# Optimization experiments

Hardware: AMD Instinct MI355X
Metric: run time of the kernel (lower is better)

Reference implementation:

```python
import jax, jax.numpy as jnp
import numpy as np

N, B, H, C, NF = 200000, 100, 128, 3, 128


def setup_inputs() -> dict:
    key = jax.random.key(0)
    ks = jax.random.split(key, 12)
    def w(k, shape, s=0.05):
        return jax.random.normal(k, shape, jnp.float32) * s
    return dict(
        node_feat=w(ks[0], (N, NF), 1.0),
        coord=w(ks[1], (N, 3), 1.0),
        virtual_node_feat=w(ks[2], (B, NF, C), 1.0),
        virtual_coord=w(ks[3], (B, 3, C), 1.0),
        data_batch=jnp.sort(jax.random.randint(ks[4], (N,), 0, B)),
        We1=w(ks[5], (2 * NF + 1, H)), be1=jnp.zeros((H,), jnp.float32),
        We2=w(ks[6], (H, H)), be2=jnp.zeros((H,), jnp.float32),
        Wc1=w(ks[7], (H, H)), bc1=jnp.zeros((H,), jnp.float32),
        Wc2=w(ks[8], (H, 1), 0.001),  # xavier gain=0.001 layer, no bias
        Wn1=w(ks[9], (2 * H, H)), bn1=jnp.zeros((H,), jnp.float32),
        Wn2=w(ks[10], (H, H)), bn2=jnp.zeros((H,), jnp.float32),
    )


def _segment_mean(x, idx, num_segments):
    # x: [N, d1, d2] -> [num_segments, d1, d2]; mean over nodes of each graph
    sums = jax.ops.segment_sum(x, idx, num_segments=num_segments)
    counts = jax.ops.segment_sum(jnp.ones((x.shape[0],), x.dtype), idx,
                                 num_segments=num_segments)
    return sums / jnp.maximum(counts, 1.0)[:, None, None]


def reference(node_feat, coord, virtual_node_feat, virtual_coord, data_batch,
              We1, be1, We2, be2, Wc1, bc1, Wc2, Wn1, bn1, Wn2, bn2):
    silu = jax.nn.silu
    n, nf = node_feat.shape
    nb, _, c = virtual_coord.shape

    # gather: real node -> its graph's virtual nodes
    diff = virtual_coord[data_batch] - coord[:, :, None]            # [N,3,C]
    radial = jnp.linalg.norm(diff, axis=1)                          # [N,C]

    # edge model (work in [N,C,feat] layout to avoid permutes)
    feat_R = jnp.broadcast_to(node_feat[:, None, :], (n, c, nf))    # [N,C,NF]
    feat_V = virtual_node_feat[data_batch].transpose(0, 2, 1)       # [N,C,NF]
    e_in = jnp.concatenate([feat_R, feat_V, radial[:, :, None]], axis=-1)
    m = silu(e_in @ We1 + be1)
    m = silu(m @ We2 + be2)                                         # [N,C,H]

    # coord model: per (node, virtual-channel) scalar weight
    s = silu(m @ Wc1 + bc1) @ Wc2                                   # [N,C,1]
    trans = diff * s[:, :, 0][:, None, :]                           # [N,3,C]
    virtual_coord = virtual_coord + _segment_mean(trans, data_batch, nb)

    # node model on virtual nodes
    agg = _segment_mean(m, data_batch, nb)                          # [B,C,H]
    n_in = jnp.concatenate([virtual_node_feat.transpose(0, 2, 1), agg], axis=-1)
    h = silu(n_in @ Wn1 + bn1) @ Wn2 + bn2                          # [B,C,H]
    virtual_node_feat = virtual_node_feat + h.transpose(0, 2, 1)    # residual

    return virtual_node_feat, virtual_coord
```

## Files before the change

### kernel.cpp

```cpp
#include <hip/hip_runtime.h>
#include <hip/hip_bf16.h>
#include <math.h>

#define NNODES 200000
#define NGRAPH 100
#define HD     128
#define NCH    3
#define BN     64
#define EROWS  (BN*NCH)
#define ESTR   136

typedef short short8 __attribute__((ext_vector_type(8)));
typedef float f32x4  __attribute__((ext_vector_type(4)));

#define MFMA_16x16x32(a,b,c) __builtin_amdgcn_mfma_f32_16x16x32_bf16((a),(b),(c),0,0,0)

__device__ __forceinline__ float bf2f(unsigned short u) {
    return __uint_as_float(((unsigned int)u) << 16);
}
__device__ __forceinline__ unsigned short f2bf(float f) {
    return (unsigned short)((__float_as_uint(f) + 0x8000u) >> 16);
}
__device__ __forceinline__ float silu_f(float x) {
    return x * __builtin_amdgcn_rcpf(1.0f + __expf(-x));
}

__global__ void prep_kernel(const float* __restrict__ We1,
                            const float* __restrict__ We2,
                            const float* __restrict__ Wc1,
                            const float* __restrict__ be1,
                            const float* __restrict__ be2,
                            const float* __restrict__ bc1,
                            const float* __restrict__ Wc2,
                            const float* __restrict__ vnf,
                            unsigned short* __restrict__ w1r,
                            unsigned short* __restrict__ w2r,
                            unsigned short* __restrict__ wc1r,
                            float* __restrict__ Q,
                            float* __restrict__ wlast,
                            float* __restrict__ be1f,
                            float* __restrict__ be2f,
                            float* __restrict__ bc1f,
                            float* __restrict__ wc2f) {
    int bid = blockIdx.x;
    if (bid < 192) {
        int t = bid * 256 + threadIdx.x;
        int m  = t / 16384;
        int e  = t % 16384;
        int j  = e & 7;
        int l  = (e >> 3) & 63;
        int ks = (e >> 9) & 3;
        int ct = e >> 11;
        int row = ks * 32 + (l >> 4) * 8 + j;
        int col = ct * 16 + (l & 15);
        const float*    src = (m == 0) ? We1 : ((m == 1) ? We2 : Wc1);
        unsigned short* dst = (m == 0) ? w1r : ((m == 1) ? w2r : wc1r);
        dst[e] = f2bf(src[row * 128 + col]);
        if (t < 128) {
            wlast[t] = We1[256 * 128 + t];
            be1f[t]  = be1[t];
            be2f[t]  = be2[t];
            bc1f[t]  = bc1[t];
            wc2f[t]  = Wc2[t];
        }
    } else {
        int bc = bid - 192;
        int b = bc / NCH, c = bc % NCH;
        int t = threadIdx.x;
        __shared__ float v[128];
        if (t < 128) v[t] = vnf[(b * 128 + t) * 3 + c];
        __syncthreads();
        if (t < 128) {
            float s = 0.0f;
            for (int k = 0; k < 128; ++k)
                s += v[k] * We1[(128 + k) * 128 + t];
            Q[(b * 3 + c) * 128 + t] = s;
        }
    }
}

__global__ __launch_bounds__(256, 2) void egcl_main(
    const float* __restrict__ node_feat,
    const float* __restrict__ coord,
    const float* __restrict__ vcoord,
    const int*   __restrict__ batch,
    const unsigned short* __restrict__ w1r,
    const unsigned short* __restrict__ w2r,
    const unsigned short* __restrict__ wc1r,
    const float* __restrict__ Q,
    const float* __restrict__ wlast,
    const float* __restrict__ be1f,
    const float* __restrict__ be2f,
    const float* __restrict__ bc1f,
    const float* __restrict__ wc2f,
    float* __restrict__ aggsum,
    float* __restrict__ transsum,
    float* __restrict__ cnt)
{
    __shared__ __align__(16) unsigned short e_buf[EROWS * ESTR];
    __shared__ float s_s[EROWS];
    __shared__ unsigned short sbatch[BN];
    __shared__ unsigned short sseg_start[BN + 1];
    __shared__ unsigned short sseg_b[BN];
    __shared__ int snseg;

    const int tid   = threadIdx.x;
    const int wave  = tid >> 6;
    const int lane  = tid & 63;
    const int lrow  = lane & 15;
    const int lkb   = (lane >> 4) * 8;
    const int rq    = (lane >> 4) * 4;
    const int node0 = blockIdx.x * BN;

    if (tid < BN) {
        int n = node0 + tid;
        int b = batch[n];
        sbatch[tid] = (unsigned short)b;
        int prev = (tid > 0) ? batch[n - 1] : -1;
        unsigned long long mask = __ballot(b != prev);
        int ns = __popcll(mask);
        if (b != prev) {
            int idx = __popcll(mask & ((1ull << tid) - 1ull));
            sseg_start[idx] = (unsigned short)tid;
            sseg_b[idx]     = (unsigned short)b;
        }
        if (tid == 0) { sseg_start[ns] = BN; snseg = ns; }
        float cx = coord[n * 3 + 0];
        float cy = coord[n * 3 + 1];
        float cz = coord[n * 3 + 2];
        for (int c = 0; c < 3; ++c) {
            float dx = vcoord[b * 9 + 0 * 3 + c] - cx;
            float dy = vcoord[b * 9 + 1 * 3 + c] - cy;
            float dz = vcoord[b * 9 + 2 * 3 + c] - cz;
            f32x4 pad;
            pad[0] = dx; pad[1] = dy; pad[2] = dz;
            pad[3] = sqrtf(dx * dx + dy * dy + dz * dz);
            *(f32x4*)&e_buf[(c * 64 + tid) * ESTR + 128] = pad;
        }
    }
    __syncthreads();
    const int nseg = snseg;

    f32x4 acc1[8] = {};
    {
        const float* arow = node_feat + (size_t)(node0 + wave * 16 + lrow) * 128;
        for (int ks = 0; ks < 4; ++ks) {
            f32x4 x0 = *(const f32x4*)(arow + ks * 32 + lkb);
            f32x4 x1 = *(const f32x4*)(arow + ks * 32 + lkb + 4);
            short8 af;
            af[0] = (short)f2bf(x0[0]); af[1] = (short)f2bf(x0[1]);
            af[2] = (short)f2bf(x0[2]); af[3] = (short)f2bf(x0[3]);
            af[4] = (short)f2bf(x1[0]); af[5] = (short)f2bf(x1[1]);
            af[6] = (short)f2bf(x1[2]); af[7] = (short)f2bf(x1[3]);
            for (int ct = 0; ct < 8; ++ct) {
                short8 bfg = *(const short8*)(w1r + ((ct * 4 + ks) * 64 + lane) * 8);
                acc1[ct] = MFMA_16x16x32(af, bfg, acc1[ct]);
            }
        }
    }
    {
        float wl[8], bb[8];
        #pragma unroll
        for (int ct = 0; ct < 8; ++ct) {
            wl[ct] = wlast[ct * 16 + lrow];
            bb[ct] = be1f[ct * 16 + lrow];
        }
        if (nseg == 1) {
            const float* qb = Q + (int)sseg_b[0] * (NCH * HD);
            float qv[3][8];
            #pragma unroll
            for (int c = 0; c < 3; ++c)
                #pragma unroll
                for (int ct = 0; ct < 8; ++ct)
                    qv[c][ct] = qb[c * 128 + ct * 16 + lrow];
            #pragma unroll
            for (int r = 0; r < 4; ++r) {
                int nl = wave * 16 + rq + r;
                #pragma unroll
                for (int c = 0; c < 3; ++c) {
                    int row = c * 64 + nl;
                    float rad = *(const float*)&e_buf[row * ESTR + 134];
                    #pragma unroll
                    for (int ct = 0; ct < 8; ++ct) {
                        float x = acc1[ct][r] + bb[ct] + qv[c][ct] + rad * wl[ct];
                        e_buf[row * ESTR + ct * 16 + lrow] = f2bf(silu_f(x));
                    }
                }
            }
        } else {
            #pragma unroll
            for (int r = 0; r < 4; ++r) {
                int nl = wave * 16 + rq + r;
                int b  = sbatch[nl];
                #pragma unroll
                for (int c = 0; c < 3; ++c) {
                    int row = c * 64 + nl;
                    float rad = *(const float*)&e_buf[row * ESTR + 134];
                    const float* qb = Q + (b * 3 + c) * 128;
                    #pragma unroll
                    for (int ct = 0; ct < 8; ++ct) {
                        float x = acc1[ct][r] + bb[ct] + qb[ct * 16 + lrow] + rad * wl[ct];
                        e_buf[row * ESTR + ct * 16 + lrow] = f2bf(silu_f(x));
                    }
                }
            }
        }
    }

    f32x4 acc2[3][8] = {};
    for (int ks = 0; ks < 4; ++ks) {
        short8 af[3];
        for (int j = 0; j < 3; ++j)
            af[j] = *(const short8*)(&e_buf[(j * 64 + wave * 16 + lrow) * ESTR +
                                            ks * 32 + lkb]);
        for (int ct = 0; ct < 8; ++ct) {
            short8 bfg = *(const short8*)(w2r + ((ct * 4 + ks) * 64 + lane) * 8);
            for (int j = 0; j < 3; ++j)
                acc2[j][ct] = MFMA_16x16x32(af[j], bfg, acc2[j][ct]);
        }
    }
    {
        const int bagg = (nseg == 1) ? (int)sseg_b[0] * (NCH * HD) : 0;
        for (int j = 0; j < 3; ++j) {
            for (int ct = 0; ct < 8; ++ct) {
                int h = ct * 16 + lrow;
                float bb = be2f[h];
                float psum = 0.0f;
                #pragma unroll
                for (int r = 0; r < 4; ++r) {
                    int row = j * 64 + wave * 16 + rq + r;
                    float v = silu_f(acc2[j][ct][r] + bb);
                    e_buf[row * ESTR + h] = f2bf(v);
                    psum += v;
                }
                if (nseg == 1) {
                    psum += __shfl_xor(psum, 16, 64);
                    psum += __shfl_xor(psum, 32, 64);
                    if (lane < 16)
                        atomicAdd(&aggsum[bagg + j * 128 + ct * 16 + lane], psum);
                }
            }
        }
    }

    f32x4 acc3[3][8] = {};
    for (int ks = 0; ks < 4; ++ks) {
        short8 af[3];
        for (int j = 0; j < 3; ++j)
            af[j] = *(const short8*)(&e_buf[(j * 64 + wave * 16 + lrow) * ESTR +
                                            ks * 32 + lkb]);
        for (int ct = 0; ct < 8; ++ct) {
            short8 bfg = *(const short8*)(wc1r + ((ct * 4 + ks) * 64 + lane) * 8);
            for (int j = 0; j < 3; ++j)
                acc3[j][ct] = MFMA_16x16x32(af[j], bfg, acc3[j][ct]);
        }
    }
    for (int j = 0; j < 3; ++j) {
        float p0 = 0.f, p1 = 0.f, p2 = 0.f, p3 = 0.f;
        for (int ct = 0; ct < 8; ++ct) {
            int h = ct * 16 + lrow;
            float bb = bc1f[h];
            float w2 = wc2f[h];
            p0 += silu_f(acc3[j][ct][0] + bb) * w2;
            p1 += silu_f(acc3[j][ct][1] + bb) * w2;
            p2 += silu_f(acc3[j][ct][2] + bb) * w2;
            p3 += silu_f(acc3[j][ct][3] + bb) * w2;
        }
        #pragma unroll
        for (int off = 1; off < 16; off <<= 1) {
            p0 += __shfl_xor(p0, off, 64);
            p1 += __shfl_xor(p1, off, 64);
            p2 += __shfl_xor(p2, off, 64);
            p3 += __shfl_xor(p3, off, 64);
        }
        if (lrow == 0) {
            int rbase = j * 64 + wave * 16 + rq;
            s_s[rbase + 0] = p0;
            s_s[rbase + 1] = p1;
            s_s[rbase + 2] = p2;
            s_s[rbase + 3] = p3;
        }
    }
    __syncthreads();

    if (nseg == 1) {
        int b = sseg_b[0];
        if (wave == 0) {
            float t[9];
            #pragma unroll
            for (int c = 0; c < 3; ++c) {
                int row = c * 64 + lane;
                float sv = s_s[row];
                float dx = *(const float*)&e_buf[row * ESTR + 128];
                float dy = *(const float*)&e_buf[row * ESTR + 130];
                float dz = *(const float*)&e_buf[row * ESTR + 132];
                t[0 * 3 + c] = dx * sv;
                t[1 * 3 + c] = dy * sv;
                t[2 * 3 + c] = dz * sv;
            }
            #pragma unroll
            for (int off = 1; off < 64; off <<= 1)
                #pragma unroll
                for (int k = 0; k < 9; ++k)
                    t[k] += __shfl_xor(t[k], off, 64);
            if (lane < 9)
                atomicAdd(&transsum[b * 9 + lane],
                          __shfl(t[lane], 0, 64));
            if (lane == 0) atomicAdd(&cnt[b], 64.0f);
        }
    } else {
        for (int sg = 0; sg < nseg; ++sg) {
            int s0 = sseg_start[sg], s1 = sseg_start[sg + 1], b = sseg_b[sg];
            for (int idx = tid; idx < NCH * HD; idx += 256) {
                int c = idx >> 7, h = idx & 127;
                float sum = 0.f;
                for (int ii = s0; ii < s1; ++ii)
                    sum += bf2f(e_buf[(c * 64 + ii) * ESTR + h]);
                atomicAdd(&aggsum[(b * 3 + c) * 128 + h], sum);
            }
            if (tid < 9) {
                int d = tid / 3, c = tid % 3;
                float sum = 0.f;
                for (int ii = s0; ii < s1; ++ii)
                    sum += (*(const float*)&e_buf[(c * 64 + ii) * ESTR + 128 + 2 * d])
                           * s_s[c * 64 + ii];
                atomicAdd(&transsum[b * 9 + d * 3 + c], sum);
            }
            if (tid == 0) atomicAdd(&cnt[b], (float)(s1 - s0));
        }
    }
}

__global__ void finalize_kernel(const float* __restrict__ vnf,
                                const float* __restrict__ vcoord,
                                const float* __restrict__ Wn1,
                                const float* __restrict__ bn1,
                                const float* __restrict__ Wn2,
                                const float* __restrict__ bn2,
                                const float* __restrict__ aggsum,
                                const float* __restrict__ transsum,
                                const float* __restrict__ cnt,
                                float* __restrict__ out) {
    int b = blockIdx.x / NCH;
    int c = blockIdx.x % NCH;
    int j = threadIdx.x;
    __shared__ float nin[256];
    __shared__ float h1[128];
    float count = fmaxf(cnt[b], 1.0f);
    nin[j]       = vnf[(b * 128 + j) * 3 + c];
    nin[128 + j] = aggsum[(b * 3 + c) * 128 + j] / count;
    __syncthreads();
    float x = bn1[j];
    for (int k = 0; k < 256; ++k)
        x += nin[k] * Wn1[k * 128 + j];
    h1[j] = silu_f(x);
    __syncthreads();
    float y = bn2[j];
    for (int k = 0; k < 128; ++k)
        y += h1[k] * Wn2[k * 128 + j];
    out[(b * 128 + j) * 3 + c] = vnf[(b * 128 + j) * 3 + c] + y;
    if (c == 0 && j < 9) {
        out[NGRAPH * 128 * 3 + b * 9 + j] =
            vcoord[b * 9 + j] + transsum[b * 9 + j] / count;
    }
}

extern "C" void kernel_launch(void* const* d_in, const int* in_sizes, int n_in,
                              void* d_out, int out_size, void* d_ws, size_t ws_size,
                              hipStream_t stream) {
    const float* node_feat = (const float*)d_in[0];
    const float* coord     = (const float*)d_in[1];
    const float* vnf       = (const float*)d_in[2];
    const float* vcoord    = (const float*)d_in[3];
    const int*   batch     = (const int*)d_in[4];
    const float* We1 = (const float*)d_in[5];
    const float* be1 = (const float*)d_in[6];
    const float* We2 = (const float*)d_in[7];
    const float* be2 = (const float*)d_in[8];
    const float* Wc1 = (const float*)d_in[9];
    const float* bc1 = (const float*)d_in[10];
    const float* Wc2 = (const float*)d_in[11];
    const float* Wn1 = (const float*)d_in[12];
    const float* bn1 = (const float*)d_in[13];
    const float* Wn2 = (const float*)d_in[14];
    const float* bn2 = (const float*)d_in[15];

    char* ws = (char*)d_ws;
    float*          aggsum   = (float*)(ws + 0);
    float*          transsum = (float*)(ws + 153600);
    float*          cntp     = (float*)(ws + 157200);
    float*          Q        = (float*)(ws + 157600);
    unsigned short* w1r      = (unsigned short*)(ws + 311200);
    unsigned short* w2r      = (unsigned short*)(ws + 343968);
    unsigned short* wc1r     = (unsigned short*)(ws + 376736);
    float*          wlast    = (float*)(ws + 409504);
    float*          be1f     = (float*)(ws + 410016);
    float*          be2f     = (float*)(ws + 410528);
    float*          bc1f     = (float*)(ws + 411040);
    float*          wc2f     = (float*)(ws + 411552);

    (void)hipMemsetAsync(d_ws, 0, 157600, stream);

    prep_kernel<<<192 + NGRAPH * NCH, 256, 0, stream>>>(
        We1, We2, Wc1, be1, be2, bc1, Wc2, vnf,
        w1r, w2r, wc1r, Q, wlast, be1f, be2f, bc1f, wc2f);

    egcl_main<<<NNODES / BN, 256, 0, stream>>>(
        node_feat, coord, vcoord, batch, w1r, w2r, wc1r, Q,
        wlast, be1f, be2f, bc1f, wc2f, aggsum, transsum, cntp);

    finalize_kernel<<<NGRAPH * NCH, 128, 0, stream>>>(
        vnf, vcoord, Wn1, bn1, Wn2, bn2, aggsum, transsum, cntp,
        (float*)d_out);
}
```

Baseline: 363.4 us.

## Process virtual channels sequentially to shrink LDS and registers, raise occupancy

Restructures the main kernel to loop over the three virtual channels one at a time instead of keeping all three channels' accumulators and LDS rows live at once. The shared edge buffer shrinks to one channel, and diff/radial values move to a separate small LDS array. Launch bounds rise from 2 to 4 blocks per CU. The aim is lower register and LDS pressure so more waves stay resident to hide latency. In exchange, each channel reloads the W2/Wc1 fragments, MFMA work is split into smaller batches with less instruction-level parallelism, and extra barriers are added for multi-segment blocks.

```diff
diff --git a/kernel.cpp b/kernel.cpp
--- a/kernel.cpp
+++ b/kernel.cpp
@@ -7,8 +7,8 @@
 #define HD     128
 #define NCH    3
 #define BN     64
-#define EROWS  (BN*NCH)
 #define ESTR   136
+
 
 typedef short short8 __attribute__((ext_vector_type(8)));
 typedef float f32x4  __attribute__((ext_vector_type(4)));
@@ -79,7 +79,7 @@
     }
 }
 
-__global__ __launch_bounds__(256, 2) void egcl_main(
+__global__ __launch_bounds__(256, 4) void egcl_main(
     const float* __restrict__ node_feat,
     const float* __restrict__ coord,
     const float* __restrict__ vcoord,
@@ -97,8 +97,9 @@
     float* __restrict__ transsum,
     float* __restrict__ cnt)
 {
-    __shared__ __align__(16) unsigned short e_buf[EROWS * ESTR];
-    __shared__ float s_s[EROWS];
+    __shared__ __align__(16) unsigned short e_buf[BN * ESTR];
+    __shared__ __align__(16) f32x4 sdr[NCH][BN];
+    __shared__ float s_s[NCH * BN];
     __shared__ unsigned short sbatch[BN];
     __shared__ unsigned short sseg_start[BN + 1];
     __shared__ unsigned short sseg_b[BN];
@@ -129,13 +130,12 @@
         float cy = coord[n * 3 + 1];
         float cz = coord[n * 3 + 2];
         for (int c = 0; c < 3; ++c) {
-            float dx = vcoord[b * 9 + 0 * 3 + c] - cx;
-            float dy = vcoord[b * 9 + 1 * 3 + c] - cy;
-            float dz = vcoord[b * 9 + 2 * 3 + c] - cz;
             f32x4 pad;
-            pad[0] = dx; pad[1] = dy; pad[2] = dz;
-            pad[3] = sqrtf(dx * dx + dy * dy + dz * dz);
-            *(f32x4*)&e_buf[(c * 64 + tid) * ESTR + 128] = pad;
+            pad[0] = vcoord[b * 9 + 0 * 3 + c] - cx;
+            pad[1] = vcoord[b * 9 + 1 * 3 + c] - cy;
+            pad[2] = vcoord[b * 9 + 2 * 3 + c] - cz;
+            pad[3] = sqrtf(pad[0]*pad[0] + pad[1]*pad[1] + pad[2]*pad[2]);
+            sdr[c][tid] = pad;
         }
     }
     __syncthreads();
@@ -158,33 +158,30 @@
             }
         }
     }
-    {
-        float wl[8], bb[8];
-        #pragma unroll
-        for (int ct = 0; ct < 8; ++ct) {
-            wl[ct] = wlast[ct * 16 + lrow];
-            bb[ct] = be1f[ct * 16 + lrow];
-        }
+
+    float wl[8], bb1[8];
+    #pragma unroll
+    for (int ct = 0; ct < 8; ++ct) {
+        wl[ct]  = wlast[ct * 16 + lrow];
+        bb1[ct] = be1f[ct * 16 + lrow];
+    }
+    const int b0   = (int)sseg_b[0];
+    const int bagg = b0 * (NCH * HD);
+
+    for (int c = 0; c < 3; ++c) {
         if (nseg == 1) {
-            const float* qb = Q + (int)sseg_b[0] * (NCH * HD);
-            float qv[3][8];
-            #pragma unroll
-            for (int c = 0; c < 3; ++c)
-                #pragma unroll
-                for (int ct = 0; ct < 8; ++ct)
-                    qv[c][ct] = qb[c * 128 + ct * 16 + lrow];
+            const float* qb = Q + bagg + c * 128;
+            float qv[8];
+            #pragma unroll
+            for (int ct = 0; ct < 8; ++ct) qv[ct] = qb[ct * 16 + lrow];
             #pragma unroll
             for (int r = 0; r < 4; ++r) {
                 int nl = wave * 16 + rq + r;
+                float rad = sdr[c][nl][3];
                 #pragma unroll
-                for (int c = 0; c < 3; ++c) {
-                    int row = c * 64 + nl;
-                    float rad = *(const float*)&e_buf[row * ESTR + 134];
-                    #pragma unroll
-                    for (int ct = 0; ct < 8; ++ct) {
-                        float x = acc1[ct][r] + bb[ct] + qv[c][ct] + rad * wl[ct];
-                        e_buf[row * ESTR + ct * 16 + lrow] = f2bf(silu_f(x));
-                    }
+                for (int ct = 0; ct < 8; ++ct) {
+                    float x = acc1[ct][r] + bb1[ct] + qv[ct] + rad * wl[ct];
+                    e_buf[nl * ESTR + ct * 16 + lrow] = f2bf(silu_f(x));
                 }
             }
         } else {
@@ -192,44 +189,34 @@
             for (int r = 0; r < 4; ++r) {
                 int nl = wave * 16 + rq + r;
                 int b  = sbatch[nl];
+                float rad = sdr[c][nl][3];
+                const float* qb = Q + (b * 3 + c) * 128;
                 #pragma unroll
-                for (int c = 0; c < 3; ++c) {
-                    int row = c * 64 + nl;
-                    float rad = *(const float*)&e_buf[row * ESTR + 134];
-                    const float* qb = Q + (b * 3 + c) * 128;
-                    #pragma unroll
-                    for (int ct = 0; ct < 8; ++ct) {
-                        float x = acc1[ct][r] + bb[ct] + qb[ct * 16 + lrow] + rad * wl[ct];
-                        e_buf[row * ESTR + ct * 16 + lrow] = f2bf(silu_f(x));
-                    }
-                }
-            }
-        }
-    }
-
-    f32x4 acc2[3][8] = {};
-    for (int ks = 0; ks < 4; ++ks) {
-        short8 af[3];
-        for (int j = 0; j < 3; ++j)
-            af[j] = *(const short8*)(&e_buf[(j * 64 + wave * 16 + lrow) * ESTR +
-                                            ks * 32 + lkb]);
-        for (int ct = 0; ct < 8; ++ct) {
-            short8 bfg = *(const short8*)(w2r + ((ct * 4 + ks) * 64 + lane) * 8);
-            for (int j = 0; j < 3; ++j)
-                acc2[j][ct] = MFMA_16x16x32(af[j], bfg, acc2[j][ct]);
-        }
-    }
-    {
-        const int bagg = (nseg == 1) ? (int)sseg_b[0] * (NCH * HD) : 0;
-        for (int j = 0; j < 3; ++j) {
+                for (int ct = 0; ct < 8; ++ct) {
+                    float x = acc1[ct][r] + bb1[ct] + qb[ct * 16 + lrow] + rad * wl[ct];
+                    e_buf[nl * ESTR + ct * 16 + lrow] = f2bf(silu_f(x));
+                }
+            }
+        }
+
+        {
+            f32x4 acc[8] = {};
+            for (int ks = 0; ks < 4; ++ks) {
+                short8 af = *(const short8*)(&e_buf[(wave * 16 + lrow) * ESTR +
+                                                    ks * 32 + lkb]);
+                for (int ct = 0; ct < 8; ++ct) {
+                    short8 bfg = *(const short8*)(w2r + ((ct * 4 + ks) * 64 + lane) * 8);
+                    acc[ct] = MFMA_16x16x32(af, bfg, acc[ct]);
+                }
+            }
             for (int ct = 0; ct < 8; ++ct) {
                 int h = ct * 16 + lrow;
                 float bb = be2f[h];
                 float psum = 0.0f;
                 #pragma unroll
                 for (int r = 0; r < 4; ++r) {
-                    int row = j * 64 + wave * 16 + rq + r;
-                    float v = silu_f(acc2[j][ct][r] + bb);
+                    int row = wave * 16 + rq + r;
+                    float v = silu_f(acc[ct][r] + bb);
                     e_buf[row * ESTR + h] = f2bf(v);
                     psum += v;
                 }
@@ -237,93 +224,95 @@
                     psum += __shfl_xor(psum, 16, 64);
                     psum += __shfl_xor(psum, 32, 64);
                     if (lane < 16)
-                        atomicAdd(&aggsum[bagg + j * 128 + ct * 16 + lane], psum);
-                }
-            }
-        }
-    }
-
-    f32x4 acc3[3][8] = {};
-    for (int ks = 0; ks < 4; ++ks) {
-        short8 af[3];
-        for (int j = 0; j < 3; ++j)
-            af[j] = *(const short8*)(&e_buf[(j * 64 + wave * 16 + lrow) * ESTR +
-                                            ks * 32 + lkb]);
-        for (int ct = 0; ct < 8; ++ct) {
-            short8 bfg = *(const short8*)(wc1r + ((ct * 4 + ks) * 64 + lane) * 8);
-            for (int j = 0; j < 3; ++j)
-                acc3[j][ct] = MFMA_16x16x32(af[j], bfg, acc3[j][ct]);
-        }
-    }
-    for (int j = 0; j < 3; ++j) {
-        float p0 = 0.f, p1 = 0.f, p2 = 0.f, p3 = 0.f;
-        for (int ct = 0; ct < 8; ++ct) {
-            int h = ct * 16 + lrow;
-            float bb = bc1f[h];
-            float w2 = wc2f[h];
-            p0 += silu_f(acc3[j][ct][0] + bb) * w2;
-            p1 += silu_f(acc3[j][ct][1] + bb) * w2;
-            p2 += silu_f(acc3[j][ct][2] + bb) * w2;
-            p3 += silu_f(acc3[j][ct][3] + bb) * w2;
-        }
-        #pragma unroll
-        for (int off = 1; off < 16; off <<= 1) {
-            p0 += __shfl_xor(p0, off, 64);
-            p1 += __shfl_xor(p1, off, 64);
-            p2 += __shfl_xor(p2, off, 64);
-            p3 += __shfl_xor(p3, off, 64);
-        }
-        if (lrow == 0) {
-            int rbase = j * 64 + wave * 16 + rq;
-            s_s[rbase + 0] = p0;
-            s_s[rbase + 1] = p1;
-            s_s[rbase + 2] = p2;
-            s_s[rbase + 3] = p3;
-        }
+                        atomicAdd(&aggsum[bagg + c * 128 + ct * 16 + lane], psum);
+                }
+            }
+        }
+
+        if (nseg > 1) {
+            __syncthreads();
+            for (int sg = 0; sg < nseg; ++sg) {
+                int s0 = sseg_start[sg], s1 = sseg_start[sg + 1], b = sseg_b[sg];
+                for (int h = tid; h < HD; h += 256) {
+                    float sum = 0.f;
+                    for (int ii = s0; ii < s1; ++ii)
+                        sum += bf2f(e_buf[ii * ESTR + h]);
+                    atomicAdd(&aggsum[(b * 3 + c) * 128 + h], sum);
+                }
+            }
+        }
+
+        {
+            f32x4 acc[8] = {};
+            for (int ks = 0; ks < 4; ++ks) {
+                short8 af = *(const short8*)(&e_buf[(wave * 16 + lrow) * ESTR +
+                                                    ks * 32 + lkb]);
+                for (int ct = 0; ct < 8; ++ct) {
+                    short8 bfg = *(const short8*)(wc1r + ((ct * 4 + ks) * 64 + lane) * 8);
+                    acc[ct] = MFMA_16x16x32(af, bfg, acc[ct]);
+                }
+            }
+            float p0 = 0.f, p1 = 0.f, p2 = 0.f, p3 = 0.f;
+            for (int ct = 0; ct < 8; ++ct) {
+                int h = ct * 16 + lrow;
+                float bb = bc1f[h];
+                float w2 = wc2f[h];
+                p0 += silu_f(acc[ct][0] + bb) * w2;
+                p1 += silu_f(acc[ct][1] + bb) * w2;
+                p2 += silu_f(acc[ct][2] + bb) * w2;
+                p3 += silu_f(acc[ct][3] + bb) * w2;
+            }
+            #pragma unroll
+            for (int off = 1; off < 16; off <<= 1) {
+                p0 += __shfl_xor(p0, off, 64);
+                p1 += __shfl_xor(p1, off, 64);
+                p2 += __shfl_xor(p2, off, 64);
+                p3 += __shfl_xor(p3, off, 64);
+            }
+            if (lrow == 0) {
+                int rbase = c * 64 + wave * 16 + rq;
+                s_s[rbase + 0] = p0;
+                s_s[rbase + 1] = p1;
+                s_s[rbase + 2] = p2;
+                s_s[rbase + 3] = p3;
+            }
+        }
+
+        if (nseg > 1) __syncthreads();
     }
     __syncthreads();
 
     if (nseg == 1) {
-        int b = sseg_b[0];
         if (wave == 0) {
             float t[9];
             #pragma unroll
             for (int c = 0; c < 3; ++c) {
-                int row = c * 64 + lane;
-                float sv = s_s[row];
-                float dx = *(const float*)&e_buf[row * ESTR + 128];
-                float dy = *(const float*)&e_buf[row * ESTR + 130];
-                float dz = *(const float*)&e_buf[row * ESTR + 132];
-                t[0 * 3 + c] = dx * sv;
-                t[1 * 3 + c] = dy * sv;
-                t[2 * 3 + c] = dz * sv;
+                float sv = s_s[c * 64 + lane];
+                f32x4 d  = sdr[c][lane];
+                t[0 * 3 + c] = d[0] * sv;
+                t[1 * 3 + c] = d[1] * sv;
+                t[2 * 3 + c] = d[2] * sv;
             }
             #pragma unroll
             for (int off = 1; off < 64; off <<= 1)
                 #pragma unroll
                 for (int k = 0; k < 9; ++k)
                     t[k] += __shfl_xor(t[k], off, 64);
-            if (lane < 9)
-                atomicAdd(&transsum[b * 9 + lane],
-                          __shfl(t[lane], 0, 64));
-            if (lane == 0) atomicAdd(&cnt[b], 64.0f);
+            if (lane == 0) {
+                #pragma unroll
+                for (int k = 0; k < 9; ++k)
+                    atomicAdd(&transsum[b0 * 9 + k], t[k]);
+                atomicAdd(&cnt[b0], 64.0f);
+            }
         }
     } else {
         for (int sg = 0; sg < nseg; ++sg) {
             int s0 = sseg_start[sg], s1 = sseg_start[sg + 1], b = sseg_b[sg];
-            for (int idx = tid; idx < NCH * HD; idx += 256) {
-                int c = idx >> 7, h = idx & 127;
-                float sum = 0.f;
-                for (int ii = s0; ii < s1; ++ii)
-                    sum += bf2f(e_buf[(c * 64 + ii) * ESTR + h]);
-                atomicAdd(&aggsum[(b * 3 + c) * 128 + h], sum);
-            }
             if (tid < 9) {
                 int d = tid / 3, c = tid % 3;
                 float sum = 0.f;
                 for (int ii = s0; ii < s1; ++ii)
-                    sum += (*(const float*)&e_buf[(c * 64 + ii) * ESTR + 128 + 2 * d])
-                           * s_s[c * 64 + ii];
+                    sum += sdr[c][ii][d] * s_s[c * 64 + ii];
                 atomicAdd(&transsum[b * 9 + d * 3 + c], sum);
             }
             if (tid == 0) atomicAdd(&cnt[b], (float)(s1 - s0));
```

After: 990.6 us. +172.6%, slower.
